# Kernel tuning notes

Measured on AMD Instinct MI355X. Metric: run time of the kernel, lower is better.

The kernel has to match this reference:

```python
import jax, jax.numpy as jnp
import numpy as np

N_HEADS = 16
WINDOW = 128
EPS = 1e-6
NEG_INF = -1e30  # effectively -inf after softmax in fp32


def setup_inputs() -> dict:
    key = jax.random.key(0)
    ks = jax.random.split(key, 5)
    B, T, D = 2, 2048, 1024
    scale = 1.0 / np.sqrt(D)
    return {
        "x": jax.random.normal(ks[0], (B, T, D), dtype=jnp.float32),
        "Wq": jax.random.normal(ks[1], (D, D), dtype=jnp.float32) * scale,
        "Wk": jax.random.normal(ks[2], (D, D), dtype=jnp.float32) * scale,
        "Wv": jax.random.normal(ks[3], (D, D), dtype=jnp.float32) * scale,
        "Wo": jax.random.normal(ks[4], (D, D), dtype=jnp.float32) * scale,
    }


def _l2norm(t):
    # torch F.normalize: t / max(||t||, eps)
    n = jnp.sqrt(jnp.sum(t * t, axis=-1, keepdims=True))
    return t / jnp.maximum(n, EPS)


def reference(x, Wq, Wk, Wv, Wo):
    B, T, D = x.shape
    H, hd = N_HEADS, D // N_HEADS
    # projections (torch Linear: x @ W.T), split heads -> [B, H, T, hd]
    def proj(W):
        return jnp.einsum('btd,ed->bte', x, W).reshape(B, T, H, hd).transpose(0, 2, 1, 3)
    q = _l2norm(proj(Wq))
    k = _l2norm(proj(Wk))
    v = proj(Wv)
    # scores [B, H, T, T] (no 1/sqrt(d) scale in the source)
    attn = jnp.einsum('bhqd,bhkd->bhqk', q, k)
    pos = jnp.arange(T)
    rel = pos[None, :] - pos[:, None]            # rel[i, j] = j - i
    mask = (rel < 0) | (rel >= WINDOW)           # allowed: 0 <= j-i < window
    base = jnp.linspace(0.0, 1.0, H, dtype=x.dtype)
    slopes = jnp.power(jnp.asarray(2.0, x.dtype), -(8.0 * base))  # [H]
    alibi = -jnp.abs(rel).astype(x.dtype)[None, :, :] * slopes[:, None, None]  # [H,T,T]
    bias = jnp.where(mask[None, :, :], jnp.asarray(NEG_INF, x.dtype), alibi)
    attn = jax.nn.softmax(attn + bias[None], axis=-1)
    out = jnp.einsum('bhqk,bhkd->bhqd', attn, v)
    out = out.transpose(0, 2, 1, 3).reshape(B, T, D)
    return jnp.einsum('btd,ed->bte', out, Wo)
```

## Files before the change

kernel.cpp:

```cpp
#include <hip/hip_runtime.h>
#include <hip/hip_bf16.h>

#define T_SEQ   2048
#define BATCH   2
#define DMODEL  1024
#define NHEADS  16
#define HDIM    64
#define WINDOW  128

typedef __attribute__((ext_vector_type(8))) short bf16x8;
typedef __attribute__((ext_vector_type(4))) float f32x4;

__device__ inline void unpack8(uint4 u, float* f) {
    unsigned int w[4] = {u.x, u.y, u.z, u.w};
#pragma unroll
    for (int i = 0; i < 4; i++) {
        f[2*i]   = __uint_as_float(w[i] << 16);
        f[2*i+1] = __uint_as_float(w[i] & 0xffff0000u);
    }
}

__device__ inline void gld_lds16(const __hip_bfloat16* g, __hip_bfloat16* l) {
    __builtin_amdgcn_global_load_lds(
        (const __attribute__((address_space(1))) unsigned int*)g,
        (__attribute__((address_space(3))) unsigned int*)l, 16, 0, 0);
}

__global__ __launch_bounds__(256) void cvt_kernel(
    const float* __restrict__ x,  const float* __restrict__ Wq,
    const float* __restrict__ Wk, const float* __restrict__ Wv,
    const float* __restrict__ Wo,
    __hip_bfloat16* __restrict__ xb, __hip_bfloat16* __restrict__ Wb)
{
    const int slot = blockIdx.y;
    const float* src;
    __hip_bfloat16* dst;
    int n;
    if (slot == 0) { src = x; dst = xb; n = 4 * 1024 * 1024; }
    else {
        src = (slot == 1) ? Wq : (slot == 2) ? Wk : (slot == 3) ? Wv : Wo;
        dst = Wb + (size_t)(slot - 1) * 1024 * 1024;
        n = 1024 * 1024;
    }
    int i = (blockIdx.x * 256 + threadIdx.x) * 8;
    if (i >= n) return;
    float4 a = *(const float4*)(src + i);
    float4 b = *(const float4*)(src + i + 4);
    __hip_bfloat16 pk[8] = {
        __float2bfloat16(a.x), __float2bfloat16(a.y),
        __float2bfloat16(a.z), __float2bfloat16(a.w),
        __float2bfloat16(b.x), __float2bfloat16(b.y),
        __float2bfloat16(b.z), __float2bfloat16(b.w)};
    *(uint4*)(dst + i) = *(uint4*)pk;
}

__global__ __launch_bounds__(256) void gemm_qkv(
    const __hip_bfloat16* __restrict__ A,
    const __hip_bfloat16* __restrict__ W0,
    const __hip_bfloat16* __restrict__ W1,
    const __hip_bfloat16* __restrict__ W2,
    __hip_bfloat16* __restrict__ C0,
    __hip_bfloat16* __restrict__ C1,
    __hip_bfloat16* __restrict__ C2,
    int M, int N, int K)
{
    const int lid   = blockIdx.x + 8 * blockIdx.y + 256 * blockIdx.z;
    const int xcd   = lid & 7;
    const int s     = lid >> 3;
    const int m_loc = s & 7;
    const int rest  = s >> 3;
    const int n_loc = rest & 3;
    const int z     = rest >> 2;

    const __hip_bfloat16* W = (z == 0) ? W0 : (z == 1 ? W1 : W2);
    __hip_bfloat16* C = (z == 0) ? C0 : (z == 1 ? C1 : C2);

    const int m0 = ((xcd & 3) * 8 + m_loc) * 128;
    const int n0 = ((xcd >> 2) * 4 + n_loc) * 128;

    __shared__ __hip_bfloat16 As[128 * 32];
    __shared__ __hip_bfloat16 Bs[128 * 32];

    const int t    = threadIdx.x;
    const int lane = t & 63;
    const int wv   = t >> 6;

    const int gc   = ((lane & 3) - (lane >> 3)) & 3;
    const int srow = wv * 32 + (lane >> 2);
    const __hip_bfloat16* Ag = A + (size_t)(m0 + srow) * K + gc * 8;
    const __hip_bfloat16* Wg = W + (size_t)(n0 + srow) * K + gc * 8;
    const size_t row16 = (size_t)16 * K;
    __hip_bfloat16* AsD0 = &As[(wv * 32) * 32];
    __hip_bfloat16* AsD1 = &As[(wv * 32 + 16) * 32];
    __hip_bfloat16* BsD0 = &Bs[(wv * 32) * 32];
    __hip_bfloat16* BsD1 = &Bs[(wv * 32 + 16) * 32];

    const int wm   = (wv >> 1) * 64;
    const int wn   = (wv & 1) * 64;
    const int lrow = lane & 15;
    const int quad = lane >> 4;
    const int slot = ((quad + (lrow >> 1)) & 3) * 8;

    f32x4 acc[4][4];
#pragma unroll
    for (int i = 0; i < 4; i++)
#pragma unroll
        for (int j = 0; j < 4; j++)
            acc[i][j] = (f32x4){0.f, 0.f, 0.f, 0.f};

    for (int k0 = 0; k0 < K; k0 += 32) {
        gld_lds16(Ag + k0,         AsD0);
        gld_lds16(Ag + k0 + row16, AsD1);
        gld_lds16(Wg + k0,         BsD0);
        gld_lds16(Wg + k0 + row16, BsD1);
        __syncthreads();

        bf16x8 af[4], bfv[4];
#pragma unroll
        for (int mi = 0; mi < 4; mi++)
            af[mi] = *(const bf16x8*)&As[(wm + mi * 16 + lrow) * 32 + slot];
#pragma unroll
        for (int ni = 0; ni < 4; ni++)
            bfv[ni] = *(const bf16x8*)&Bs[(wn + ni * 16 + lrow) * 32 + slot];
#pragma unroll
        for (int mi = 0; mi < 4; mi++)
#pragma unroll
            for (int ni = 0; ni < 4; ni++)
                acc[mi][ni] = __builtin_amdgcn_mfma_f32_16x16x32_bf16(
                    af[mi], bfv[ni], acc[mi][ni], 0, 0, 0);
        __syncthreads();
    }

    if (z != 2) {
#pragma unroll
        for (int mi = 0; mi < 4; mi++) {
#pragma unroll
            for (int rr = 0; rr < 4; rr++) {
                float ss = 0.f;
#pragma unroll
                for (int ni = 0; ni < 4; ni++)
                    ss += acc[mi][ni][rr] * acc[mi][ni][rr];
                ss += __shfl_xor(ss, 1);
                ss += __shfl_xor(ss, 2);
                ss += __shfl_xor(ss, 4);
                ss += __shfl_xor(ss, 8);
                float inv = 1.0f / fmaxf(sqrtf(ss), 1e-6f);
#pragma unroll
                for (int ni = 0; ni < 4; ni++)
                    acc[mi][ni][rr] *= inv;
            }
        }
    }

#pragma unroll
    for (int mi = 0; mi < 4; mi++) {
#pragma unroll
        for (int rr = 0; rr < 4; rr++) {
            int row = m0 + wm + mi * 16 + quad * 4 + rr;
            __hip_bfloat16* Crow = C + (size_t)row * N + n0 + wn + lrow;
#pragma unroll
            for (int ni = 0; ni < 4; ni++)
                Crow[ni * 16] = __float2bfloat16(acc[mi][ni][rr]);
        }
    }
}

__global__ __launch_bounds__(256) void gemm_o(
    const __hip_bfloat16* __restrict__ A,
    const __hip_bfloat16* __restrict__ W,
    float* __restrict__ C,
    int M, int N, int K)
{
    const int lid   = blockIdx.x + 8 * blockIdx.y;
    const int xcd   = lid & 7;
    const int s     = lid >> 3;
    const int m_loc = s & 15;
    const int n_loc = s >> 4;

    const int m0 = ((xcd & 3) * 16 + m_loc) * 64;
    const int n0 = ((xcd >> 2) * 4 + n_loc) * 128;

    __shared__ __hip_bfloat16 As[64 * 32];
    __shared__ __hip_bfloat16 Bs[128 * 32];

    const int t    = threadIdx.x;
    const int lane = t & 63;
    const int wv   = t >> 6;

    const int gc    = ((lane & 3) - (lane >> 3)) & 3;
    const int srowA = wv * 16 + (lane >> 2);
    const int srowB = wv * 32 + (lane >> 2);
    const __hip_bfloat16* Ag = A + (size_t)(m0 + srowA) * K + gc * 8;
    const __hip_bfloat16* Wg = W + (size_t)(n0 + srowB) * K + gc * 8;
    const size_t row16 = (size_t)16 * K;
    __hip_bfloat16* AsD0 = &As[(wv * 16) * 32];
    __hip_bfloat16* BsD0 = &Bs[(wv * 32) * 32];
    __hip_bfloat16* BsD1 = &Bs[(wv * 32 + 16) * 32];

    const int wm   = (wv >> 1) * 32;
    const int wn   = (wv & 1) * 64;
    const int lrow = lane & 15;
    const int quad = lane >> 4;
    const int slot = ((quad + (lrow >> 1)) & 3) * 8;

    f32x4 acc[2][4];
#pragma unroll
    for (int i = 0; i < 2; i++)
#pragma unroll
        for (int j = 0; j < 4; j++)
            acc[i][j] = (f32x4){0.f, 0.f, 0.f, 0.f};

    for (int k0 = 0; k0 < K; k0 += 32) {
        gld_lds16(Ag + k0, AsD0);
        gld_lds16(Wg + k0,         BsD0);
        gld_lds16(Wg + k0 + row16, BsD1);
        __syncthreads();

        bf16x8 af[2], bfv[4];
#pragma unroll
        for (int mi = 0; mi < 2; mi++)
            af[mi] = *(const bf16x8*)&As[(wm + mi * 16 + lrow) * 32 + slot];
#pragma unroll
        for (int ni = 0; ni < 4; ni++)
            bfv[ni] = *(const bf16x8*)&Bs[(wn + ni * 16 + lrow) * 32 + slot];
#pragma unroll
        for (int mi = 0; mi < 2; mi++)
#pragma unroll
            for (int ni = 0; ni < 4; ni++)
                acc[mi][ni] = __builtin_amdgcn_mfma_f32_16x16x32_bf16(
                    af[mi], bfv[ni], acc[mi][ni], 0, 0, 0);
        __syncthreads();
    }

#pragma unroll
    for (int mi = 0; mi < 2; mi++) {
#pragma unroll
        for (int rr = 0; rr < 4; rr++) {
            int row = m0 + wm + mi * 16 + quad * 4 + rr;
            float* Crow = C + (size_t)row * N + n0 + wn + lrow;
#pragma unroll
            for (int ni = 0; ni < 4; ni++)
                Crow[ni * 16] = acc[mi][ni][rr];
        }
    }
}

__global__ __launch_bounds__(256) void attn_kernel(
    const __hip_bfloat16* __restrict__ Q,
    const __hip_bfloat16* __restrict__ K,
    const __hip_bfloat16* __restrict__ V,
    __hip_bfloat16* __restrict__ O)
{
    const int i0 = blockIdx.x * 64;
    const int h  = blockIdx.y;
    const int b  = blockIdx.z;

    __shared__ __hip_bfloat16 Ks[192 * 64];
    __shared__ __hip_bfloat16 Vt[64 * 200];

    const size_t base = ((size_t)b * T_SEQ) * DMODEL + h * HDIM;
    const int t    = threadIdx.x;
    const int lane = t & 63;
    const int w    = t >> 6;

    {
        const int drow = lane >> 3, sl = lane & 7;
#pragma unroll
        for (int inst = 0; inst < 6; inst++) {
            int r0 = w * 48 + inst * 8;
            int r  = r0 + drow;
            int gcx = (sl - r) & 7;
            int j  = min(i0 + r, T_SEQ - 1);
            gld_lds16(K + base + (size_t)j * DMODEL + gcx * 8, &Ks[r0 * 64]);
        }
    }
    for (int task = t; task < 192; task += 256) {
        int c  = task & 7;
        int r0 = (task >> 3) * 8;
        int b0 = task >> 3;
        unsigned short m[8][8];
#pragma unroll
        for (int i = 0; i < 8; i++) {
            int j = min(i0 + r0 + i, T_SEQ - 1);
            uint4 u = *(const uint4*)(V + base + (size_t)j * DMODEL + c * 8);
            unsigned short tmp[8];
            *(uint4*)tmp = u;
#pragma unroll
            for (int e = 0; e < 8; e++) m[e][i] = tmp[e];
        }
#pragma unroll
        for (int e = 0; e < 8; e++) {
            int d  = c * 8 + e;
            int sg = (b0 & ~7) | ((b0 + (d >> 3)) & 7);
            *(uint4*)&Vt[d * 200 + sg * 8] = *(uint4*)m[e];
        }
    }
    for (int task = t; task < 64; task += 256) {
        uint4 zz = {0, 0, 0, 0};
        *(uint4*)&Vt[task * 200 + 192] = zz;
    }
    __syncthreads();

    const int col  = lane & 15;
    const int quad = lane >> 4;
    const float slope = exp2f(-8.0f * (float)h / 15.0f);

    const __hip_bfloat16* qp = Q + base + (size_t)(i0 + w * 16 + col) * DMODEL + quad * 8;
    bf16x8 qf0 = *(const bf16x8*)(qp);
    bf16x8 qf1 = *(const bf16x8*)(qp + 32);

    f32x4 sc[9];
#pragma unroll
    for (int kt = 0; kt < 9; kt++) {
        sc[kt] = (f32x4){0.f, 0.f, 0.f, 0.f};
        int r = w * 16 + kt * 16 + col;
        bf16x8 kb0 = *(const bf16x8*)&Ks[r * 64 + ((quad     + r) & 7) * 8];
        bf16x8 kb1 = *(const bf16x8*)&Ks[r * 64 + ((quad + 4 + r) & 7) * 8];
        sc[kt] = __builtin_amdgcn_mfma_f32_16x16x32_bf16(qf0, kb0, sc[kt], 0, 0, 0);
        sc[kt] = __builtin_amdgcn_mfma_f32_16x16x32_bf16(qf1, kb1, sc[kt], 0, 0, 0);
    }

    float mx[4] = {-3e38f, -3e38f, -3e38f, -3e38f};
#pragma unroll
    for (int kt = 0; kt < 9; kt++) {
#pragma unroll
        for (int r = 0; r < 4; r++) {
            int ql  = quad * 4 + r;
            int rel = kt * 16 + col - ql;
            int ka  = i0 + w * 16 + kt * 16 + col;
            bool valid = (rel >= 0) && (rel < WINDOW) && (ka < T_SEQ);
            float v = valid ? (sc[kt][r] - (float)rel * slope) : -1e30f;
            sc[kt][r] = v;
            mx[r] = fmaxf(mx[r], v);
        }
    }
#pragma unroll
    for (int r = 0; r < 4; r++) {
        mx[r] = fmaxf(mx[r], __shfl_xor(mx[r], 1));
        mx[r] = fmaxf(mx[r], __shfl_xor(mx[r], 2));
        mx[r] = fmaxf(mx[r], __shfl_xor(mx[r], 4));
        mx[r] = fmaxf(mx[r], __shfl_xor(mx[r], 8));
    }
    float sm[4] = {0.f, 0.f, 0.f, 0.f};
#pragma unroll
    for (int kt = 0; kt < 9; kt++) {
#pragma unroll
        for (int r = 0; r < 4; r++) {
            float e = __expf(sc[kt][r] - mx[r]);
            sc[kt][r] = e;
            sm[r] += e;
        }
    }
#pragma unroll
    for (int r = 0; r < 4; r++) {
        sm[r] += __shfl_xor(sm[r], 1);
        sm[r] += __shfl_xor(sm[r], 2);
        sm[r] += __shfl_xor(sm[r], 4);
        sm[r] += __shfl_xor(sm[r], 8);
        sm[r] = 1.0f / sm[r];
    }

    __syncthreads();
    __hip_bfloat16* Ps = Ks + w * (16 * 168);
#pragma unroll
    for (int kt = 0; kt < 9; kt++)
#pragma unroll
        for (int r = 0; r < 4; r++)
            Ps[(quad * 4 + r) * 168 + kt * 16 + col] = __float2bfloat16(sc[kt][r] * sm[r]);
#pragma unroll
    for (int i = 0; i < 4; i++)
        Ps[(lane & 15) * 168 + 144 + quad * 4 + i] = __float2bfloat16(0.f);
    __syncthreads();

    f32x4 o[4];
#pragma unroll
    for (int nd = 0; nd < 4; nd++) o[nd] = (f32x4){0.f, 0.f, 0.f, 0.f};
#pragma unroll
    for (int kc = 0; kc < 5; kc++) {
        bf16x8 pf = *(const bf16x8*)&Ps[col * 168 + kc * 32 + quad * 8];
        int bblk = w * 2 + kc * 4 + quad;
#pragma unroll
        for (int nd = 0; nd < 4; nd++) {
            int d  = nd * 16 + col;
            int sg = (bblk < 24) ? ((bblk & ~7) | ((bblk + (d >> 3)) & 7)) : 24;
            bf16x8 vf = *(const bf16x8*)&Vt[d * 200 + sg * 8];
            o[nd] = __builtin_amdgcn_mfma_f32_16x16x32_bf16(pf, vf, o[nd], 0, 0, 0);
        }
    }

#pragma unroll
    for (int r = 0; r < 4; r++) {
        __hip_bfloat16* op = O + base + (size_t)(i0 + w * 16 + quad * 4 + r) * DMODEL + col;
#pragma unroll
        for (int nd = 0; nd < 4; nd++)
            op[nd * 16] = __float2bfloat16(o[nd][r]);
    }
}

extern "C" void kernel_launch(void* const* d_in, const int* in_sizes, int n_in,
                              void* d_out, int out_size, void* d_ws, size_t ws_size,
                              hipStream_t stream)
{
    const float* x  = (const float*)d_in[0];
    const float* Wq = (const float*)d_in[1];
    const float* Wk = (const float*)d_in[2];
    const float* Wv = (const float*)d_in[3];
    const float* Wo = (const float*)d_in[4];
    float* out = (float*)d_out;

    const size_t MT = (size_t)BATCH * T_SEQ;
    __hip_bfloat16* Qw = (__hip_bfloat16*)d_ws;
    __hip_bfloat16* Kw = Qw + MT * DMODEL;
    __hip_bfloat16* Vw = Kw + MT * DMODEL;
    __hip_bfloat16* XA = Vw + MT * DMODEL;
    __hip_bfloat16* Wb = XA + MT * DMODEL;

    cvt_kernel<<<dim3(2048, 5), 256, 0, stream>>>(x, Wq, Wk, Wv, Wo, XA, Wb);

    dim3 g1(DMODEL / 128, MT / 128, 3);
    gemm_qkv<<<g1, 256, 0, stream>>>(
        XA, Wb, Wb + 1024 * 1024, Wb + 2 * 1024 * 1024,
        Qw, Kw, Vw, (int)MT, DMODEL, DMODEL);

    dim3 g2(T_SEQ / 64, NHEADS, BATCH);
    attn_kernel<<<g2, 256, 0, stream>>>(Qw, Kw, Vw, XA);

    dim3 g3(DMODEL / 128, MT / 64, 1);
    gemm_o<<<g3, 256, 0, stream>>>(
        XA, Wb + 3 * 1024 * 1024, out, (int)MT, DMODEL, DMODEL);
}
```

Measured before the change: 153.8 us.

## Widen attention query tile to 128 rows and compact the conversion grid

New measurement: 150.9 us. Within noise of the previous version (-1.8%).

```diff
diff --git a/kernel.cpp b/kernel.cpp
--- a/kernel.cpp
+++ b/kernel.cpp
@@ -11,15 +11,6 @@
 typedef __attribute__((ext_vector_type(8))) short bf16x8;
 typedef __attribute__((ext_vector_type(4))) float f32x4;
 
-__device__ inline void unpack8(uint4 u, float* f) {
-    unsigned int w[4] = {u.x, u.y, u.z, u.w};
-#pragma unroll
-    for (int i = 0; i < 4; i++) {
-        f[2*i]   = __uint_as_float(w[i] << 16);
-        f[2*i+1] = __uint_as_float(w[i] & 0xffff0000u);
-    }
-}
-
 __device__ inline void gld_lds16(const __hip_bfloat16* g, __hip_bfloat16* l) {
     __builtin_amdgcn_global_load_lds(
         (const __attribute__((address_space(1))) unsigned int*)g,
@@ -32,18 +23,18 @@
     const float* __restrict__ Wo,
     __hip_bfloat16* __restrict__ xb, __hip_bfloat16* __restrict__ Wb)
 {
-    const int slot = blockIdx.y;
+    const int lid = blockIdx.x;
     const float* src;
     __hip_bfloat16* dst;
-    int n;
-    if (slot == 0) { src = x; dst = xb; n = 4 * 1024 * 1024; }
+    int blk;
+    if (lid < 2048) { src = x; dst = xb; blk = lid; }
     else {
-        src = (slot == 1) ? Wq : (slot == 2) ? Wk : (slot == 3) ? Wv : Wo;
-        dst = Wb + (size_t)(slot - 1) * 1024 * 1024;
-        n = 1024 * 1024;
-    }
-    int i = (blockIdx.x * 256 + threadIdx.x) * 8;
-    if (i >= n) return;
+        int slot = (lid - 2048) >> 9;
+        blk = (lid - 2048) & 511;
+        src = (slot == 0) ? Wq : (slot == 1) ? Wk : (slot == 2) ? Wv : Wo;
+        dst = Wb + (size_t)slot * 1024 * 1024;
+    }
+    int i = (blk * 256 + threadIdx.x) * 8;
     float4 a = *(const float4*)(src + i);
     float4 b = *(const float4*)(src + i + 4);
     __hip_bfloat16 pk[8] = {
@@ -245,18 +236,18 @@
     }
 }
 
-__global__ __launch_bounds__(256) void attn_kernel(
+__global__ __launch_bounds__(512) void attn_kernel(
     const __hip_bfloat16* __restrict__ Q,
     const __hip_bfloat16* __restrict__ K,
     const __hip_bfloat16* __restrict__ V,
     __hip_bfloat16* __restrict__ O)
 {
-    const int i0 = blockIdx.x * 64;
+    const int qb = blockIdx.x * 128;
     const int h  = blockIdx.y;
     const int b  = blockIdx.z;
 
-    __shared__ __hip_bfloat16 Ks[192 * 64];
-    __shared__ __hip_bfloat16 Vt[64 * 200];
+    __shared__ __hip_bfloat16 KsP[8 * 16 * 168];
+    __shared__ __hip_bfloat16 Vt[64 * 264];
 
     const size_t base = ((size_t)b * T_SEQ) * DMODEL + h * HDIM;
     const int t    = threadIdx.x;
@@ -266,22 +257,22 @@
     {
         const int drow = lane >> 3, sl = lane & 7;
 #pragma unroll
-        for (int inst = 0; inst < 6; inst++) {
-            int r0 = w * 48 + inst * 8;
+        for (int inst = 0; inst < 4; inst++) {
+            int r0 = w * 32 + inst * 8;
             int r  = r0 + drow;
             int gcx = (sl - r) & 7;
-            int j  = min(i0 + r, T_SEQ - 1);
-            gld_lds16(K + base + (size_t)j * DMODEL + gcx * 8, &Ks[r0 * 64]);
-        }
-    }
-    for (int task = t; task < 192; task += 256) {
-        int c  = task & 7;
-        int r0 = (task >> 3) * 8;
-        int b0 = task >> 3;
+            int j  = min(qb + r, T_SEQ - 1);
+            gld_lds16(K + base + (size_t)j * DMODEL + gcx * 8, &KsP[r0 * 64]);
+        }
+    }
+    if (t < 256) {
+        int c  = t & 7;
+        int b0 = t >> 3;
+        int sg = (b0 & ~7) | ((b0 + c) & 7);
         unsigned short m[8][8];
 #pragma unroll
         for (int i = 0; i < 8; i++) {
-            int j = min(i0 + r0 + i, T_SEQ - 1);
+            int j = min(qb + b0 * 8 + i, T_SEQ - 1);
             uint4 u = *(const uint4*)(V + base + (size_t)j * DMODEL + c * 8);
             unsigned short tmp[8];
             *(uint4*)tmp = u;
@@ -289,15 +280,12 @@
             for (int e = 0; e < 8; e++) m[e][i] = tmp[e];
         }
 #pragma unroll
-        for (int e = 0; e < 8; e++) {
-            int d  = c * 8 + e;
-            int sg = (b0 & ~7) | ((b0 + (d >> 3)) & 7);
-            *(uint4*)&Vt[d * 200 + sg * 8] = *(uint4*)m[e];
-        }
-    }
-    for (int task = t; task < 64; task += 256) {
+        for (int e = 0; e < 8; e++)
+            *(uint4*)&Vt[(c * 8 + e) * 264 + sg * 8] = *(uint4*)m[e];
+    }
+    if (t < 64) {
         uint4 zz = {0, 0, 0, 0};
-        *(uint4*)&Vt[task * 200 + 192] = zz;
+        *(uint4*)&Vt[t * 264 + 256] = zz;
     }
     __syncthreads();
 
@@ -305,7 +293,7 @@
     const int quad = lane >> 4;
     const float slope = exp2f(-8.0f * (float)h / 15.0f);
 
-    const __hip_bfloat16* qp = Q + base + (size_t)(i0 + w * 16 + col) * DMODEL + quad * 8;
+    const __hip_bfloat16* qp = Q + base + (size_t)(qb + w * 16 + col) * DMODEL + quad * 8;
     bf16x8 qf0 = *(const bf16x8*)(qp);
     bf16x8 qf1 = *(const bf16x8*)(qp + 32);
 
@@ -314,8 +302,8 @@
     for (int kt = 0; kt < 9; kt++) {
         sc[kt] = (f32x4){0.f, 0.f, 0.f, 0.f};
         int r = w * 16 + kt * 16 + col;
-        bf16x8 kb0 = *(const bf16x8*)&Ks[r * 64 + ((quad     + r) & 7) * 8];
-        bf16x8 kb1 = *(const bf16x8*)&Ks[r * 64 + ((quad + 4 + r) & 7) * 8];
+        bf16x8 kb0 = *(const bf16x8*)&KsP[r * 64 + ((quad     + r) & 7) * 8];
+        bf16x8 kb1 = *(const bf16x8*)&KsP[r * 64 + ((quad + 4 + r) & 7) * 8];
         sc[kt] = __builtin_amdgcn_mfma_f32_16x16x32_bf16(qf0, kb0, sc[kt], 0, 0, 0);
         sc[kt] = __builtin_amdgcn_mfma_f32_16x16x32_bf16(qf1, kb1, sc[kt], 0, 0, 0);
     }
@@ -327,7 +315,7 @@
         for (int r = 0; r < 4; r++) {
             int ql  = quad * 4 + r;
             int rel = kt * 16 + col - ql;
-            int ka  = i0 + w * 16 + kt * 16 + col;
+            int ka  = qb + w * 16 + kt * 16 + col;
             bool valid = (rel >= 0) && (rel < WINDOW) && (ka < T_SEQ);
             float v = valid ? (sc[kt][r] - (float)rel * slope) : -1e30f;
             sc[kt][r] = v;
@@ -361,7 +349,7 @@
     }
 
     __syncthreads();
-    __hip_bfloat16* Ps = Ks + w * (16 * 168);
+    __hip_bfloat16* Ps = KsP + w * (16 * 168);
 #pragma unroll
     for (int kt = 0; kt < 9; kt++)
 #pragma unroll
@@ -382,15 +370,15 @@
 #pragma unroll
         for (int nd = 0; nd < 4; nd++) {
             int d  = nd * 16 + col;
-            int sg = (bblk < 24) ? ((bblk & ~7) | ((bblk + (d >> 3)) & 7)) : 24;
-            bf16x8 vf = *(const bf16x8*)&Vt[d * 200 + sg * 8];
+            int sg = (bblk < 32) ? ((bblk & ~7) | ((bblk + (d >> 3)) & 7)) : 32;
+            bf16x8 vf = *(const bf16x8*)&Vt[d * 264 + sg * 8];
             o[nd] = __builtin_amdgcn_mfma_f32_16x16x32_bf16(pf, vf, o[nd], 0, 0, 0);
         }
     }
 
 #pragma unroll
     for (int r = 0; r < 4; r++) {
-        __hip_bfloat16* op = O + base + (size_t)(i0 + w * 16 + quad * 4 + r) * DMODEL + col;
+        __hip_bfloat16* op = O + base + (size_t)(qb + w * 16 + quad * 4 + r) * DMODEL + col;
 #pragma unroll
         for (int nd = 0; nd < 4; nd++)
             op[nd * 16] = __float2bfloat16(o[nd][r]);
@@ -415,15 +403,15 @@
     __hip_bfloat16* XA = Vw + MT * DMODEL;
     __hip_bfloat16* Wb = XA + MT * DMODEL;
 
-    cvt_kernel<<<dim3(2048, 5), 256, 0, stream>>>(x, Wq, Wk, Wv, Wo, XA, Wb);
+    cvt_kernel<<<4096, 256, 0, stream>>>(x, Wq, Wk, Wv, Wo, XA, Wb);
 
     dim3 g1(DMODEL / 128, MT / 128, 3);
     gemm_qkv<<<g1, 256, 0, stream>>>(
         XA, Wb, Wb + 1024 * 1024, Wb + 2 * 1024 * 1024,
         Qw, Kw, Vw, (int)MT, DMODEL, DMODEL);
 
-    dim3 g2(T_SEQ / 64, NHEADS, BATCH);
-    attn_kernel<<<g2, 256, 0, stream>>>(Qw, Kw, Vw, XA);
+    dim3 g2(T_SEQ / 128, NHEADS, BATCH);
+    attn_kernel<<<g2, 512, 0, stream>>>(Qw, Kw, Vw, XA);
 
     dim3 g3(DMODEL / 128, MT / 64, 1);
     gemm_o<<<g3, 256, 0, stream>>>(
```
